# Kernel optimization log

Measured on AMD Instinct MI355X. Metric: run time of the kernel, lower is better.

Reference implementation:

```python
import jax, jax.numpy as jnp
import numpy as np

B = 1024      # number of subgraphs in the batch
S = 128       # nodes per subgraph (last node is the anchor)
N = B * S     # total nodes
E = 2_097_152 # total edges (avg degree 16)
F_IN = 300
F_OUT = 64


def setup_inputs() -> dict:
    key = jax.random.key(0)
    kx, kg, ks, kd, kw = jax.random.split(key, 5)
    in_feat = jax.random.normal(kx, (N, F_IN), dtype=jnp.float32)
    # edges constrained within subgraphs (batched DGL graph semantics)
    gid = jax.random.randint(kg, (E,), 0, B)
    src = (gid * S + jax.random.randint(ks, (E,), 0, S)).astype(jnp.int32)
    dst = (gid * S + jax.random.randint(kd, (E,), 0, S)).astype(jnp.int32)
    W = jax.random.normal(kw, (F_IN, F_OUT), dtype=jnp.float32) * 0.05
    b = jnp.zeros((F_OUT,), dtype=jnp.float32)
    prelu_a = jnp.float32(0.25)  # nn.PReLU default single parameter
    return {"in_feat": in_feat, "W": W, "b": b, "prelu_a": prelu_a,
            "src": src, "dst": dst}


def reference(in_feat, W, b, prelu_a, src, dst):
    ones = jnp.ones((E,), dtype=jnp.float32)
    deg_out = jnp.clip(jax.ops.segment_sum(ones, src, num_segments=N), 1.0)
    deg_in = jnp.clip(jax.ops.segment_sum(ones, dst, num_segments=N), 1.0)
    # GraphConv norm='both': weight first (in_feats > out_feats), then SpMM
    x = in_feat * jax.lax.rsqrt(deg_out)[:, None]
    h = x @ W                                   # [N, F_OUT]
    agg = jax.ops.segment_sum(h[src], dst, num_segments=N)
    h = agg * jax.lax.rsqrt(deg_in)[:, None] + b
    # PReLU
    h = jnp.where(h > 0, h, prelu_a * h)
    # ragged per-subgraph mean over all nodes except the last (anchor)
    node_idx = jnp.arange(N)
    seg = node_idx // S                          # subgraph id per node
    not_anchor = ((node_idx % S) != (S - 1)).astype(h.dtype)
    pool_sum = jax.ops.segment_sum(h * not_anchor[:, None], seg, num_segments=B)
    subgraph_pool_emb = pool_sum / jnp.float32(S - 1)
    anchor_out = h[(jnp.arange(B) + 1) * S - 1]  # last node of each subgraph
    return subgraph_pool_emb, anchor_out
```

## Files before the change

kernel.cpp:

```cpp
#include <hip/hip_runtime.h>
#include <hip/hip_bf16.h>

#define NNODES 131072
#define NEDGES 2097152
#define BSUB   1024
#define SSUB   128
#define FIN    300
#define FOUT   64
#define NCHUNK 1024
#define CHEDGE 2048

typedef __attribute__((ext_vector_type(8))) short short8;
typedef __attribute__((ext_vector_type(8))) unsigned short ushort8;
typedef __attribute__((ext_vector_type(4))) float f32x4;

__device__ inline unsigned short f2bfbits(float f) {
    union { __hip_bfloat16 h; unsigned short u; } cv;
    cv.h = __float2bfloat16(f);
    return cv.u;
}
__device__ inline float bf2f(unsigned short b) {
    return __uint_as_float(((unsigned)b) << 16);
}

__device__ inline void gload_lds16(const float* g, void* l) {
    __builtin_amdgcn_global_load_lds(
        (const __attribute__((address_space(1))) unsigned int*)g,
        (__attribute__((address_space(3))) unsigned int*)l,
        16, 0, 0);
}

__global__ __launch_bounds__(256) void prep_w_kernel(const float* __restrict__ W,
                                                     short* __restrict__ wfrag) {
    int idx = blockIdx.x * 256 + threadIdx.x;
    if (idx >= 2560) return;
    int ct   = idx / 640;
    int rem  = idx % 640;
    int kt   = rem / 64;
    int lane = rem % 64;
    int col  = ct * 16 + (lane & 15);
    int kb   = kt * 32 + (lane >> 4) * 8;
#pragma unroll
    for (int e = 0; e < 8; ++e) {
        int k = kb + e;
        float v = (k < FIN) ? W[(size_t)k * FOUT + col] : 0.f;
        wfrag[(size_t)idx * 8 + e] = (short)f2bfbits(v);
    }
}

__global__ __launch_bounds__(256) void bucket_kernel(const int* __restrict__ src,
                                                     const int* __restrict__ dst,
                                                     unsigned* __restrict__ ofs,
                                                     unsigned short* __restrict__ bkt) {
    __shared__ unsigned short epack[CHEDGE];
    __shared__ unsigned short eg[CHEDGE];
    __shared__ unsigned short sorted[CHEDGE];
    __shared__ int hist[BSUB];
    __shared__ int cur[BSUB];
    __shared__ int wsum[4];

    const int cb = blockIdx.x;
    const int t = threadIdx.x;
    for (int i = t; i < BSUB; i += 256) hist[i] = 0;
    __syncthreads();

    const int4* sp = (const int4*)(src + (size_t)cb * CHEDGE);
    const int4* dp = (const int4*)(dst + (size_t)cb * CHEDGE);
    for (int i = t; i < CHEDGE / 4; i += 256) {
        int4 s4 = sp[i], d4 = dp[i];
#pragma unroll
        for (int k = 0; k < 4; ++k) {
            int s = (k == 0) ? s4.x : (k == 1) ? s4.y : (k == 2) ? s4.z : s4.w;
            int d = (k == 0) ? d4.x : (k == 1) ? d4.y : (k == 2) ? d4.z : d4.w;
            int g = s >> 7;
            epack[i * 4 + k] = (unsigned short)(((s & 127) << 7) | (d & 127));
            eg[i * 4 + k] = (unsigned short)g;
            atomicAdd(&hist[g], 1);
        }
    }
    __syncthreads();

    {
        int lane = t & 63, w = t >> 6;
        int c0 = hist[4 * t], c1 = hist[4 * t + 1], c2 = hist[4 * t + 2], c3 = hist[4 * t + 3];
        int s = c0 + c1 + c2 + c3;
        int pre = s;
#pragma unroll
        for (int o = 1; o < 64; o <<= 1) {
            int v = __shfl_up(pre, o, 64);
            if (lane >= o) pre += v;
        }
        if (lane == 63) wsum[w] = pre;
        __syncthreads();
        int wbase = 0;
        for (int i = 0; i < w; ++i) wbase += wsum[i];
        int excl = wbase + pre - s;
        uint4 ov;
        ov.x = ((unsigned)excl << 16) | (unsigned)c0; cur[4 * t]     = excl; excl += c0;
        ov.y = ((unsigned)excl << 16) | (unsigned)c1; cur[4 * t + 1] = excl; excl += c1;
        ov.z = ((unsigned)excl << 16) | (unsigned)c2; cur[4 * t + 2] = excl; excl += c2;
        ov.w = ((unsigned)excl << 16) | (unsigned)c3; cur[4 * t + 3] = excl;
        ((uint4*)(ofs + (size_t)cb * BSUB))[t] = ov;
    }
    __syncthreads();

    for (int i = t; i < CHEDGE; i += 256) {
        int g = eg[i];
        int r = atomicAdd(&cur[g], 1);
        sorted[r] = epack[i];
    }
    __syncthreads();

    {
        ushort8* outv = (ushort8*)(bkt + (size_t)cb * CHEDGE);
        const ushort8* sv = (const ushort8*)sorted;
        for (int i = t; i < CHEDGE / 8; i += 256) outv[i] = sv[i];
    }
}

__global__ __launch_bounds__(256, 2) void gemm_kernel(const float* __restrict__ x,
                                                      const short* __restrict__ wfrag,
                                                      unsigned short* __restrict__ hb) {
    __shared__ __align__(16) char smem[77824];
    char* bufA = smem;
    char* bufB = smem + 32768;
    char* aux  = smem + 65536;

    const int wave = threadIdx.x >> 6;
    const int lane = threadIdx.x & 63;
    const int rowbase = blockIdx.x * 64;

    short8 bq[10];
#pragma unroll
    for (int kt = 0; kt < 10; ++kt)
        bq[kt] = *(const short8*)(wfrag + ((size_t)(wave * 10 + kt) * 64 + lane) * 8);

#pragma unroll
    for (int i = wave; i < 32; i += 4) {
        int o = i * 1024 + lane * 16;
        int row = o >> 9;
        int c = o & 511;
        int csrc = c ^ ((row & 7) << 4);
        gload_lds16(x + (size_t)(rowbase + row) * FIN + (csrc >> 2), bufA + i * 1024);
    }
#pragma unroll
    for (int i = wave; i < 32; i += 4) {
        int o = i * 1024 + lane * 16;
        int row = o >> 9;
        int c = o & 511;
        int csrc = c ^ ((row & 7) << 4);
        gload_lds16(x + (size_t)(rowbase + row) * FIN + 128 + (csrc >> 2), bufB + i * 1024);
    }
    for (int i = wave; i < 11; i += 4) {
        int o = i * 1024 + lane * 16;
        int row = o / 176;
        int c = o - row * 176;
        gload_lds16(x + (size_t)(rowbase + row) * FIN + 256 + (c >> 2), aux + i * 1024);
    }
    ((float*)(aux + 11264))[threadIdx.x] = 0.f;

    f32x4 acc[4];
#pragma unroll
    for (int r = 0; r < 4; ++r) acc[r] = (f32x4){0.f, 0.f, 0.f, 0.f};

    const int kg = lane >> 4;

    __syncthreads();

#pragma unroll
    for (int rt = 0; rt < 4; ++rt) {
        const int rl = rt * 16 + (lane & 15);
        const int sw = (rl & 7) << 4;
#pragma unroll
        for (int kt = 0; kt < 10; ++kt) {
            f32x4 lo, hi;
            if (kt < 8) {
                const char* buf = (kt < 4) ? bufA : bufB;
                int c0 = (kt & 3) * 128 + kg * 32;
                lo = *(const f32x4*)(buf + rl * 512 + (c0 ^ sw));
                hi = *(const f32x4*)(buf + rl * 512 + ((c0 + 16) ^ sw));
            } else {
                int c0 = (kt - 8) * 128 + kg * 32;
                lo = *(const f32x4*)(aux + rl * 176 + c0);
                hi = *(const f32x4*)(aux + rl * 176 + c0 + 16);
            }
            short8 afr;
            afr[0] = (short)f2bfbits(lo[0]); afr[1] = (short)f2bfbits(lo[1]);
            afr[2] = (short)f2bfbits(lo[2]); afr[3] = (short)f2bfbits(lo[3]);
            afr[4] = (short)f2bfbits(hi[0]); afr[5] = (short)f2bfbits(hi[1]);
            afr[6] = (short)f2bfbits(hi[2]); afr[7] = (short)f2bfbits(hi[3]);
            acc[rt] = __builtin_amdgcn_mfma_f32_16x16x32_bf16(afr, bq[kt], acc[rt], 0, 0, 0);
        }
    }

    __syncthreads();

    {
        unsigned short* st = (unsigned short*)aux;
        const int colb = wave * 16 + (lane & 15);
#pragma unroll
        for (int rt = 0; rt < 4; ++rt) {
            const int rbase = rt * 16 + (lane >> 4) * 4;
#pragma unroll
            for (int r = 0; r < 4; ++r)
                st[(rbase + r) * FOUT + colb] = f2bfbits(acc[rt][r]);
        }
        __syncthreads();
        const ushort8* sv = (const ushort8*)st;
        ushort8* hout = (ushort8*)(hb + (size_t)rowbase * FOUT);
        hout[threadIdx.x] = sv[threadIdx.x];
        hout[threadIdx.x + 256] = sv[threadIdx.x + 256];
    }
}

__global__ __launch_bounds__(256) void agg_pool_kernel(const unsigned short* __restrict__ hb,
                                                       const unsigned short* __restrict__ bkt,
                                                       const unsigned* __restrict__ ofs,
                                                       const float* __restrict__ bias,
                                                       const float* __restrict__ prelu,
                                                       float* __restrict__ out) {
    __shared__ unsigned short hl[SSUB][FOUT];
    __shared__ unsigned short el[4096];
    __shared__ unsigned char  es[SSUB][64];
    __shared__ int   din[SSUB];
    __shared__ int   dout[SSUB];
    __shared__ float rout[SSUB];
    __shared__ float ps[4][FOUT];
    __shared__ int   wsum[4];

    const int g = blockIdx.x;
    const int t = threadIdx.x;
    const int lane = t & 63;
    const int w = t >> 6;

    unsigned w32[4];
    int rst[4], cn[4];
    int mycnt = 0;
#pragma unroll
    for (int j = 0; j < 4; ++j) {
        w32[j] = ofs[(size_t)(4 * t + j) * BSUB + g];
        rst[j] = (int)(w32[j] >> 16);
        cn[j] = (int)(w32[j] & 0xffff);
        mycnt += cn[j];
    }
    int pre = mycnt;
#pragma unroll
    for (int o = 1; o < 64; o <<= 1) {
        int v = __shfl_up(pre, o, 64);
        if (lane >= o) pre += v;
    }
    if (lane == 63) wsum[w] = pre;

    {
        const ushort8* hsrc = (const ushort8*)(hb + (size_t)g * SSUB * FOUT);
        ushort8* hdst = (ushort8*)&hl[0][0];
        for (int i = t; i < 1024; i += 256) hdst[i] = hsrc[i];
    }
    if (t < SSUB) { din[t] = 0; dout[t] = 0; }
    __syncthreads();

    int wbase = 0;
    for (int i = 0; i < w; ++i) wbase += wsum[i];
    int myoff = wbase + pre - mycnt;
    const int cnt = wsum[0] + wsum[1] + wsum[2] + wsum[3];

    {
        int o = myoff;
#pragma unroll
        for (int j = 0; j < 4; ++j) {
            const unsigned short* ebb = bkt + ((size_t)(4 * t + j) << 11) + rst[j];
            int lim = min(cn[j], 4096 - o);
            for (int i = 0; i < lim; ++i) el[o + i] = ebb[i];
            o += lim;
        }
    }
    __syncthreads();

    for (int i = t; i < cnt; i += 256) {
        unsigned e = el[i];
        int s = e >> 7, d = e & 127;
        int r = atomicAdd(&din[d], 1);
        es[d][r & 63] = (unsigned char)s;
        atomicAdd(&dout[s], 1);
    }
    __syncthreads();
    if (t < SSUB) rout[t] = rsqrtf((float)max(dout[t], 1));
    __syncthreads();

    const float bv = bias[lane];
    const float a = prelu[0];
    float pool = 0.f;
#pragma unroll 4
    for (int ii = 0; ii < 32; ++ii) {
        int d = w + 4 * ii;
        int cd = min(din[d], 64);
        float accv = 0.f;
        const unsigned* ew = (const unsigned*)&es[d][0];
        int nw = (cd + 3) >> 2;
        for (int p = 0; p < nw; ++p) {
            unsigned wd = ew[p];
            int rem = cd - p * 4;
#pragma unroll
            for (int b = 0; b < 4; ++b) {
                if (b < rem) {
                    int s = (wd >> (8 * b)) & 127;
                    accv += bf2f(hl[s][lane]) * rout[s];
                }
            }
        }
        float v = accv * rsqrtf((float)max(din[d], 1)) + bv;
        v = (v > 0.f) ? v : a * v;
        if (d == SSUB - 1)
            out[(size_t)(BSUB + g) * FOUT + lane] = v;
        else
            pool += v;
    }
    ps[w][lane] = pool;
    __syncthreads();
    if (w == 0) {
        float s = (ps[0][lane] + ps[1][lane]) + (ps[2][lane] + ps[3][lane]);
        out[(size_t)g * FOUT + lane] = s * (1.0f / 127.0f);
    }
}

extern "C" void kernel_launch(void* const* d_in, const int* in_sizes, int n_in,
                              void* d_out, int out_size, void* d_ws, size_t ws_size,
                              hipStream_t stream) {
    const float* in_feat = (const float*)d_in[0];
    const float* W       = (const float*)d_in[1];
    const float* bias    = (const float*)d_in[2];
    const float* prelu   = (const float*)d_in[3];
    const int*   src     = (const int*)d_in[4];
    const int*   dst     = (const int*)d_in[5];
    float* out = (float*)d_out;

    char* ws = (char*)d_ws;
    short*          wfrag = (short*)(ws + 65536);
    unsigned*       ofs   = (unsigned*)(ws + (2u << 20));
    unsigned short* bkt   = (unsigned short*)(ws + (8u << 20));
    unsigned short* hb    = (unsigned short*)(ws + (16u << 20));

    hipLaunchKernelGGL(prep_w_kernel,   dim3(10),        dim3(256), 0, stream, W, wfrag);
    hipLaunchKernelGGL(bucket_kernel,   dim3(NCHUNK),    dim3(256), 0, stream, src, dst, ofs, bkt);
    hipLaunchKernelGGL(gemm_kernel,     dim3(NNODES/64), dim3(256), 0, stream, in_feat, wfrag, hb);
    hipLaunchKernelGGL(agg_pool_kernel, dim3(BSUB),      dim3(256), 0, stream, hb, bkt, ofs, bias, prelu, out);
}
```

Before: 113.5 us.

## Merge bucket and GEMM kernels into one launch, build W fragments inline

Combines the edge-bucketing kernel and the GEMM kernel into a single launch, with the block index choosing which role a block plays, so the two independent stages can run concurrently on the GPU. The separate W-preparation kernel is removed; each GEMM block now loads W and converts it to bf16 fragments itself. This cuts two kernel launches and lets bucketing overlap the GEMM, but every GEMM block repeats strided scalar loads of W, and the bucket path now runs under the larger GEMM shared-memory footprint and launch bounds.

```diff
diff --git a/kernel.cpp b/kernel.cpp
--- a/kernel.cpp
+++ b/kernel.cpp
@@ -30,110 +30,90 @@
         16, 0, 0);
 }
 
-__global__ __launch_bounds__(256) void prep_w_kernel(const float* __restrict__ W,
-                                                     short* __restrict__ wfrag) {
-    int idx = blockIdx.x * 256 + threadIdx.x;
-    if (idx >= 2560) return;
-    int ct   = idx / 640;
-    int rem  = idx % 640;
-    int kt   = rem / 64;
-    int lane = rem % 64;
-    int col  = ct * 16 + (lane & 15);
-    int kb   = kt * 32 + (lane >> 4) * 8;
-#pragma unroll
-    for (int e = 0; e < 8; ++e) {
-        int k = kb + e;
-        float v = (k < FIN) ? W[(size_t)k * FOUT + col] : 0.f;
-        wfrag[(size_t)idx * 8 + e] = (short)f2bfbits(v);
-    }
-}
-
-__global__ __launch_bounds__(256) void bucket_kernel(const int* __restrict__ src,
-                                                     const int* __restrict__ dst,
-                                                     unsigned* __restrict__ ofs,
-                                                     unsigned short* __restrict__ bkt) {
-    __shared__ unsigned short epack[CHEDGE];
-    __shared__ unsigned short eg[CHEDGE];
-    __shared__ unsigned short sorted[CHEDGE];
-    __shared__ int hist[BSUB];
-    __shared__ int cur[BSUB];
-    __shared__ int wsum[4];
-
-    const int cb = blockIdx.x;
-    const int t = threadIdx.x;
-    for (int i = t; i < BSUB; i += 256) hist[i] = 0;
-    __syncthreads();
-
-    const int4* sp = (const int4*)(src + (size_t)cb * CHEDGE);
-    const int4* dp = (const int4*)(dst + (size_t)cb * CHEDGE);
-    for (int i = t; i < CHEDGE / 4; i += 256) {
-        int4 s4 = sp[i], d4 = dp[i];
-#pragma unroll
-        for (int k = 0; k < 4; ++k) {
-            int s = (k == 0) ? s4.x : (k == 1) ? s4.y : (k == 2) ? s4.z : s4.w;
-            int d = (k == 0) ? d4.x : (k == 1) ? d4.y : (k == 2) ? d4.z : d4.w;
-            int g = s >> 7;
-            epack[i * 4 + k] = (unsigned short)(((s & 127) << 7) | (d & 127));
-            eg[i * 4 + k] = (unsigned short)g;
-            atomicAdd(&hist[g], 1);
-        }
-    }
-    __syncthreads();
-
-    {
-        int lane = t & 63, w = t >> 6;
-        int c0 = hist[4 * t], c1 = hist[4 * t + 1], c2 = hist[4 * t + 2], c3 = hist[4 * t + 3];
-        int s = c0 + c1 + c2 + c3;
-        int pre = s;
-#pragma unroll
-        for (int o = 1; o < 64; o <<= 1) {
-            int v = __shfl_up(pre, o, 64);
-            if (lane >= o) pre += v;
-        }
-        if (lane == 63) wsum[w] = pre;
-        __syncthreads();
-        int wbase = 0;
-        for (int i = 0; i < w; ++i) wbase += wsum[i];
-        int excl = wbase + pre - s;
-        uint4 ov;
-        ov.x = ((unsigned)excl << 16) | (unsigned)c0; cur[4 * t]     = excl; excl += c0;
-        ov.y = ((unsigned)excl << 16) | (unsigned)c1; cur[4 * t + 1] = excl; excl += c1;
-        ov.z = ((unsigned)excl << 16) | (unsigned)c2; cur[4 * t + 2] = excl; excl += c2;
-        ov.w = ((unsigned)excl << 16) | (unsigned)c3; cur[4 * t + 3] = excl;
-        ((uint4*)(ofs + (size_t)cb * BSUB))[t] = ov;
-    }
-    __syncthreads();
-
-    for (int i = t; i < CHEDGE; i += 256) {
-        int g = eg[i];
-        int r = atomicAdd(&cur[g], 1);
-        sorted[r] = epack[i];
-    }
-    __syncthreads();
-
-    {
-        ushort8* outv = (ushort8*)(bkt + (size_t)cb * CHEDGE);
-        const ushort8* sv = (const ushort8*)sorted;
-        for (int i = t; i < CHEDGE / 8; i += 256) outv[i] = sv[i];
-    }
-}
-
-__global__ __launch_bounds__(256, 2) void gemm_kernel(const float* __restrict__ x,
-                                                      const short* __restrict__ wfrag,
-                                                      unsigned short* __restrict__ hb) {
+__global__ __launch_bounds__(256, 2) void front_kernel(const int* __restrict__ src,
+                                                       const int* __restrict__ dst,
+                                                       unsigned* __restrict__ ofs,
+                                                       unsigned short* __restrict__ bkt,
+                                                       const float* __restrict__ x,
+                                                       const float* __restrict__ W,
+                                                       unsigned short* __restrict__ hb) {
     __shared__ __align__(16) char smem[77824];
+
+    if (blockIdx.x < NCHUNK) {
+        unsigned short* epack  = (unsigned short*)smem;
+        unsigned short* eg     = (unsigned short*)(smem + 4096);
+        unsigned short* sorted = (unsigned short*)(smem + 8192);
+        int* hist = (int*)(smem + 12288);
+        int* cur  = (int*)(smem + 16384);
+        int* wsum = (int*)(smem + 20480);
+
+        const int cb = blockIdx.x;
+        const int t = threadIdx.x;
+        for (int i = t; i < BSUB; i += 256) hist[i] = 0;
+        __syncthreads();
+
+        const int4* sp = (const int4*)(src + (size_t)cb * CHEDGE);
+        const int4* dp = (const int4*)(dst + (size_t)cb * CHEDGE);
+        for (int i = t; i < CHEDGE / 4; i += 256) {
+            int4 s4 = sp[i], d4 = dp[i];
+#pragma unroll
+            for (int k = 0; k < 4; ++k) {
+                int s = (k == 0) ? s4.x : (k == 1) ? s4.y : (k == 2) ? s4.z : s4.w;
+                int d = (k == 0) ? d4.x : (k == 1) ? d4.y : (k == 2) ? d4.z : d4.w;
+                int g = s >> 7;
+                epack[i * 4 + k] = (unsigned short)(((s & 127) << 7) | (d & 127));
+                eg[i * 4 + k] = (unsigned short)g;
+                atomicAdd(&hist[g], 1);
+            }
+        }
+        __syncthreads();
+
+        {
+            int lane = t & 63, w = t >> 6;
+            int c0 = hist[4 * t], c1 = hist[4 * t + 1], c2 = hist[4 * t + 2], c3 = hist[4 * t + 3];
+            int s = c0 + c1 + c2 + c3;
+            int pre = s;
+#pragma unroll
+            for (int o = 1; o < 64; o <<= 1) {
+                int v = __shfl_up(pre, o, 64);
+                if (lane >= o) pre += v;
+            }
+            if (lane == 63) wsum[w] = pre;
+            __syncthreads();
+            int wbase = 0;
+            for (int i = 0; i < w; ++i) wbase += wsum[i];
+            int excl = wbase + pre - s;
+            uint4 ov;
+            ov.x = ((unsigned)excl << 16) | (unsigned)c0; cur[4 * t]     = excl; excl += c0;
+            ov.y = ((unsigned)excl << 16) | (unsigned)c1; cur[4 * t + 1] = excl; excl += c1;
+            ov.z = ((unsigned)excl << 16) | (unsigned)c2; cur[4 * t + 2] = excl; excl += c2;
+            ov.w = ((unsigned)excl << 16) | (unsigned)c3; cur[4 * t + 3] = excl;
+            ((uint4*)(ofs + (size_t)cb * BSUB))[t] = ov;
+        }
+        __syncthreads();
+
+        for (int i = t; i < CHEDGE; i += 256) {
+            int g = eg[i];
+            int r = atomicAdd(&cur[g], 1);
+            sorted[r] = epack[i];
+        }
+        __syncthreads();
+
+        {
+            ushort8* outv = (ushort8*)(bkt + (size_t)cb * CHEDGE);
+            const ushort8* sv = (const ushort8*)sorted;
+            for (int i = t; i < CHEDGE / 8; i += 256) outv[i] = sv[i];
+        }
+        return;
+    }
+
     char* bufA = smem;
     char* bufB = smem + 32768;
     char* aux  = smem + 65536;
 
     const int wave = threadIdx.x >> 6;
     const int lane = threadIdx.x & 63;
-    const int rowbase = blockIdx.x * 64;
-
-    short8 bq[10];
-#pragma unroll
-    for (int kt = 0; kt < 10; ++kt)
-        bq[kt] = *(const short8*)(wfrag + ((size_t)(wave * 10 + kt) * 64 + lane) * 8);
+    const int rowbase = (blockIdx.x - NCHUNK) * 64;
 
 #pragma unroll
     for (int i = wave; i < 32; i += 4) {
@@ -158,6 +138,21 @@
         gload_lds16(x + (size_t)(rowbase + row) * FIN + 256 + (c >> 2), aux + i * 1024);
     }
     ((float*)(aux + 11264))[threadIdx.x] = 0.f;
+
+    short8 bq[10];
+    {
+        const int col = wave * 16 + (lane & 15);
+        const int krow = (lane >> 4) * 8;
+#pragma unroll
+        for (int kt = 0; kt < 10; ++kt) {
+#pragma unroll
+            for (int e = 0; e < 8; ++e) {
+                int k = kt * 32 + krow + e;
+                float v = (k < FIN) ? W[(size_t)k * FOUT + col] : 0.f;
+                bq[kt][e] = (short)f2bfbits(v);
+            }
+        }
+    }
 
     f32x4 acc[4];
 #pragma unroll
@@ -335,13 +330,12 @@
     float* out = (float*)d_out;
 
     char* ws = (char*)d_ws;
-    short*          wfrag = (short*)(ws + 65536);
-    unsigned*       ofs   = (unsigned*)(ws + (2u << 20));
-    unsigned short* bkt   = (unsigned short*)(ws + (8u << 20));
-    unsigned short* hb    = (unsigned short*)(ws + (16u << 20));
-
-    hipLaunchKernelGGL(prep_w_kernel,   dim3(10),        dim3(256), 0, stream, W, wfrag);
-    hipLaunchKernelGGL(bucket_kernel,   dim3(NCHUNK),    dim3(256), 0, stream, src, dst, ofs, bkt);
-    hipLaunchKernelGGL(gemm_kernel,     dim3(NNODES/64), dim3(256), 0, stream, in_feat, wfrag, hb);
-    hipLaunchKernelGGL(agg_pool_kernel, dim3(BSUB),      dim3(256), 0, stream, hb, bkt, ofs, bias, prelu, out);
-}
+    unsigned*       ofs = (unsigned*)(ws + (2u << 20));
+    unsigned short* bkt = (unsigned short*)(ws + (8u << 20));
+    unsigned short* hb  = (unsigned short*)(ws + (16u << 20));
+
+    hipLaunchKernelGGL(front_kernel,    dim3(NCHUNK + NNODES/64), dim3(256), 0, stream,
+                       src, dst, ofs, bkt, in_feat, W, hb);
+    hipLaunchKernelGGL(agg_pool_kernel, dim3(BSUB),               dim3(256), 0, stream,
+                       hb, bkt, ofs, bias, prelu, out);
+}
```

After: 121.0 us. 6.6% more time.
